# Optimization experiments

Measured on AMD Instinct MI355X. Metric: run time of the kernel, lower is better.

The kernel has to match this reference:

```python
import jax, jax.numpy as jnp
import numpy as np

N_SRC, N_TGT, N_EDGES = 100000, 50000, 600000
IN_CH, OUT_CH = 128, 128
NUM_EDGE_TYPES, NUM_NODE_TYPES = 7, 4


def setup_inputs() -> dict:
    key = jax.random.key(0)
    ks = jax.random.split(key, 9)
    x_src = jax.random.normal(ks[0], (N_SRC, IN_CH), dtype=jnp.float32)
    x_target = jax.random.normal(ks[1], (N_TGT, IN_CH), dtype=jnp.float32)
    # PyG Linear: y = x @ W.T (+ b); W has shape (out, in)
    rel_w = jax.random.normal(ks[2], (NUM_EDGE_TYPES, OUT_CH, IN_CH), dtype=jnp.float32) * 0.05
    root_w = jax.random.normal(ks[3], (NUM_NODE_TYPES, OUT_CH, IN_CH), dtype=jnp.float32) * 0.05
    root_b = jax.random.normal(ks[4], (NUM_NODE_TYPES, OUT_CH), dtype=jnp.float32) * 0.05
    edge_src = jax.random.randint(ks[5], (N_EDGES,), 0, N_SRC, dtype=jnp.int32)
    edge_dst = jax.random.randint(ks[6], (N_EDGES,), 0, N_TGT, dtype=jnp.int32)
    edge_type = jax.random.randint(ks[7], (N_EDGES,), 0, NUM_EDGE_TYPES, dtype=jnp.int32)
    target_node_type = jax.random.randint(ks[8], (N_TGT,), 0, NUM_NODE_TYPES, dtype=jnp.int32)
    return {
        "x_src": x_src, "x_target": x_target,
        "rel_w": rel_w, "root_w": root_w, "root_b": root_b,
        "edge_src": edge_src, "edge_dst": edge_dst,
        "edge_type": edge_type, "target_node_type": target_node_type,
    }


def reference(x_src, x_target, rel_w, root_w, root_b,
              edge_src, edge_dst, edge_type, target_node_type):
    n_tgt = x_target.shape[0]
    num_rel = rel_w.shape[0]
    num_ntypes = root_w.shape[0]
    # Gather source features once for all edges: (E, in)
    msg = x_src[edge_src]
    out = jnp.zeros((n_tgt, rel_w.shape[1]), dtype=x_target.dtype)
    # Per-relation linear transform + scatter-MEAN over that relation's edges
    # (matches one propagate(aggr='mean') call per edge type: nodes with no
    #  incoming edges of type r contribute 0 for that relation).
    for r in range(num_rel):
        mask = (edge_type == r).astype(msg.dtype)  # (E,)
        y = (msg * mask[:, None]) @ rel_w[r].T     # (E, out)
        s = jax.ops.segment_sum(y, edge_dst, num_segments=n_tgt)
        cnt = jax.ops.segment_sum(mask, edge_dst, num_segments=n_tgt)
        out = out + s / jnp.maximum(cnt, 1.0)[:, None]
    # Per-node-type root linear (with bias), masked add
    for t in range(num_ntypes):
        m = (target_node_type == t)
        root = x_target @ root_w[t].T + root_b[t]
        out = out + jnp.where(m[:, None], root, 0.0)
    return out
```

## Files before the change

kernel.cpp:

```cpp
#include <hip/hip_runtime.h>

#define NSRC 100000
#define NTGT 50000
#define NE   600000
#define CH   128
#define NREL 7
#define NTYP 4
#define NP   (NREL * NTGT)
#define NB   ((NP + 1023) / 1024)
#define NBLK (NTGT / 16)

typedef __attribute__((ext_vector_type(4))) float f32x4;
typedef __attribute__((ext_vector_type(8))) short bf16x8;
typedef unsigned int uint;
typedef unsigned short ushort;

static constexpr long long NXB4 = (long long)NSRC * CH / 4;
static constexpr long long NXT4 = (long long)NTGT * CH / 4;
static constexpr long long NWR4 = (long long)NREL * CH * CH / 4;
static constexpr long long NWT4 = (long long)NTYP * CH * CH / 4;
static constexpr int CONVB  = (int)((NXB4 + NXT4 + NWR4 + NWT4 + 255) / 256);
static constexpr int COUNTB = (NE + 255) / 256;

static constexpr size_t A256(size_t x) { return (x + 255) & ~(size_t)255; }
static constexpr size_t CNT_O   = 0;
static constexpr size_t BSE_O   = A256(CNT_O + (size_t)NP * 4);
static constexpr size_t EOFF_O  = A256(BSE_O + (size_t)NB * 4);
static constexpr size_t CUR_O   = A256(EOFF_O + (size_t)(NP + 1) * 4);
static constexpr size_t SEDGE_O = A256(CUR_O + (size_t)NP * 4);
static constexpr size_t WB_O    = A256(SEDGE_O + (size_t)NE * 4);
static constexpr size_t XB_O    = A256(WB_O + (size_t)(NREL + NTYP) * CH * CH * 2);
static constexpr size_t XTB_O   = A256(XB_O + (size_t)NSRC * CH * 2);

#define GLOAD_LDS(gp, lp) __builtin_amdgcn_global_load_lds( \
    (const __attribute__((address_space(1))) void*)(gp), \
    (__attribute__((address_space(3))) void*)(lp), 16, 0, 0)
#define FENCE_VM()   asm volatile("s_waitcnt vmcnt(0)" ::: "memory")
#define FENCE_FULL() asm volatile("s_waitcnt vmcnt(0) lgkmcnt(0)" ::: "memory")

__device__ __forceinline__ uint bfpack(float a, float b) {
  uint ua = __float_as_uint(a); ua = (ua + 0x7fff + ((ua >> 16) & 1)) >> 16;
  uint ub = __float_as_uint(b); ub = (ub + 0x7fff + ((ub >> 16) & 1)) >> 16;
  return ua | (ub << 16);
}
__device__ __forceinline__ ushort f2b(float x) {
  uint u = __float_as_uint(x);
  return (ushort)((u + 0x7fff + ((u >> 16) & 1)) >> 16);
}
__device__ __forceinline__ float bl(uint u) { return __uint_as_float(u << 16); }
__device__ __forceinline__ float bh(uint u) { return __uint_as_float(u & 0xffff0000u); }

__global__ __launch_bounds__(256) void k_count(const int* __restrict__ edst,
                                               const int* __restrict__ etyp,
                                               int* __restrict__ cnt) {
  int i = blockIdx.x * 256 + threadIdx.x;
  if (i < NE) atomicAdd(&cnt[etyp[i] * NTGT + edst[i]], 1);
}

__global__ __launch_bounds__(256) void k_s1(const int* __restrict__ cnt,
                                            int* __restrict__ bsE) {
  __shared__ int sE[256];
  int t = threadIdx.x, p0 = blockIdx.x * 1024 + t * 4;
  int e = 0;
#pragma unroll
  for (int j = 0; j < 4; ++j) {
    int p = p0 + j;
    if (p < NP) e += cnt[p];
  }
  sE[t] = e; __syncthreads();
  for (int s = 128; s > 0; s >>= 1) {
    if (t < s) sE[t] += sE[t + s];
    __syncthreads();
  }
  if (t == 0) bsE[blockIdx.x] = sE[0];
}

__global__ __launch_bounds__(512) void k_s23(const int* __restrict__ cnt,
                                             const int* __restrict__ bsE,
                                             int* __restrict__ eoff,
                                             int* __restrict__ cur) {
  __shared__ int sE[512];
  __shared__ int sBase;
  int t = threadIdx.x;
  int e = (t < NB) ? bsE[t] : 0;
  sE[t] = e; __syncthreads();
  for (int s = 1; s < 512; s <<= 1) {
    int a = 0; if (t >= s) a = sE[t - s];
    __syncthreads();
    sE[t] += a;
    __syncthreads();
  }
  if (t == blockIdx.x) sBase = sE[t] - e;
  __syncthreads();
  int base0 = sBase;
  int p0 = blockIdx.x * 1024 + t * 2;
  int c0 = (p0 < NP) ? cnt[p0] : 0;
  int c1 = (p0 + 1 < NP) ? cnt[p0 + 1] : 0;
  int e2 = c0 + c1;
  sE[t] = e2; __syncthreads();
  for (int s = 1; s < 512; s <<= 1) {
    int a = 0; if (t >= s) a = sE[t - s];
    __syncthreads();
    sE[t] += a;
    __syncthreads();
  }
  int baseE = base0 + sE[t] - e2;
  if (p0 < NP)     { eoff[p0] = baseE;          cur[p0] = baseE; }
  if (p0 + 1 < NP) { eoff[p0 + 1] = baseE + c0; cur[p0 + 1] = baseE + c0; }
  if (p0 + 1 == NP - 1) eoff[NP] = baseE + c0 + c1;
}

__global__ __launch_bounds__(256) void k_esconv(
    const int* __restrict__ esrc, const int* __restrict__ edst,
    const int* __restrict__ etyp, int* __restrict__ cur, int* __restrict__ sedge,
    const float* __restrict__ xsrc, const float* __restrict__ xt,
    const float* __restrict__ relw, const float* __restrict__ rootw,
    ushort* __restrict__ xb, ushort* __restrict__ xtb, ushort* __restrict__ wb) {
  int bx = blockIdx.x;
  if (bx < COUNTB) {
    int i = bx * 256 + threadIdx.x;
    if (i < NE) {
      int p = etyp[i] * NTGT + edst[i];
      int pos = atomicAdd(&cur[p], 1);
      sedge[pos] = esrc[i];
    }
    return;
  }
  bx -= COUNTB;
  long long i4 = (long long)bx * 256 + threadIdx.x;
  const float* src; ushort* dst; long long off;
  if (i4 < NXB4) { src = xsrc; dst = xb; off = i4; }
  else if (i4 < NXB4 + NXT4) { src = xt; dst = xtb; off = i4 - NXB4; }
  else if (i4 < NXB4 + NXT4 + NWR4) { src = relw; dst = wb; off = i4 - NXB4 - NXT4; }
  else if (i4 < NXB4 + NXT4 + NWR4 + NWT4) {
    src = rootw; dst = wb + (size_t)NREL * CH * CH; off = i4 - NXB4 - NXT4 - NWR4;
  } else return;
  float4 v = *(const float4*)(src + off * 4);
  uint lo = (uint)f2b(v.x) | ((uint)f2b(v.y) << 16);
  uint hi = (uint)f2b(v.z) | ((uint)f2b(v.w) << 16);
  uint2 o = make_uint2(lo, hi);
  *(uint2*)(dst + off * 4) = o;
}

__device__ __forceinline__ void mfma_acc(const ushort* strip, const ushort* W,
                                         int m, int quad, f32x4* acc) {
  bf16x8 aF[4];
#pragma unroll
  for (int ks = 0; ks < 4; ++ks) {
    int c = ks * 4 + quad;
    aF[ks] = *(const bf16x8*)&strip[(m * 16 + (c ^ m)) << 3];
  }
#pragma unroll
  for (int ct = 0; ct < 8; ++ct) {
    int n = ct * 16 + m;
#pragma unroll
    for (int ks = 0; ks < 4; ++ks) {
      bf16x8 bF = *(const bf16x8*)(W + (size_t)n * CH + ks * 32 + quad * 8);
      acc[ct] = __builtin_amdgcn_mfma_f32_16x16x32_bf16(aF[ks], bF, acc[ct], 0, 0, 0);
    }
  }
}

__global__ __launch_bounds__(64) void k_mega(const ushort* __restrict__ xb,
    const ushort* __restrict__ xtb, const ushort* __restrict__ wb,
    const int* __restrict__ eoff, const int* __restrict__ sedge,
    const int* __restrict__ ntyp, const float* __restrict__ rootb,
    float* __restrict__ out) {
  __shared__ ushort As[16 * CH];
  int ln = threadIdx.x;
  int m = ln & 15, quad = ln >> 4;
  int dstbase = blockIdx.x * 16;

  int lc = min(ln, 16);
  int evr[NREL];
#pragma unroll
  for (int r = 0; r < NREL; ++r)
    evr[r] = eoff[r * NTGT + dstbase + lc];
  int nv = ntyp[dstbase + min(ln, 15)];
  uint xr[16];
#pragma unroll
  for (int i = 0; i < 16; ++i)
    xr[i] = *(const uint*)(xtb + (size_t)(dstbase + i) * CH + (ln << 1));

  f32x4 acc[8];
#pragma unroll
  for (int ct = 0; ct < 8; ++ct) acc[ct] = (f32x4){0.f, 0.f, 0.f, 0.f};

#pragma unroll
  for (int rel = 0; rel < NREL; ++rel) {
    int ev = evr[rel];
    int e0 = __builtin_amdgcn_readlane(ev, 0);
    int e1 = __builtin_amdgcn_readlane(ev, 16);
    if (e1 <= e0) continue;

    float aRx[16], aRy[16];
#pragma unroll
    for (int i = 0; i < 16; ++i) { aRx[i] = 0.f; aRy[i] = 0.f; }

    for (int cb = e0; cb < e1; cb += 16) {
      int nc = e1 - cb; if (nc > 16) nc = 16;
      int ng = (nc + 3) >> 2;
      uint ai[4];
      int esl = cb + (ln >> 4);
#pragma unroll
      for (int g = 0; g < 4; ++g) {
        if (g < ng) {
          int e = esl + g * 4;
          if (e > e1 - 1) e = e1 - 1;
          ai[g] = (uint)sedge[e];
        }
      }
      FENCE_FULL();
#pragma unroll
      for (int g = 0; g < 4; ++g) {
        if (g < ng) {
          const ushort* gp = xb + (size_t)ai[g] * CH + ((ln & 15) << 3);
          GLOAD_LDS(gp, &As[g << 9]);
        }
      }
      FENCE_VM();
#pragma unroll
      for (int i = 0; i < 16; ++i) {
        int lo = __builtin_amdgcn_readlane(ev, i);
        int hi = __builtin_amdgcn_readlane(ev, i + 1);
        if (lo < cb) lo = cb;
        int ce = cb + nc; if (hi > ce) hi = ce;
        for (int e = lo; e < hi; ++e) {
          uint u = *(const uint*)&As[((e - cb) << 7) + (ln << 1)];
          aRx[i] += bl(u);
          aRy[i] += bh(u);
        }
      }
    }

#pragma unroll
    for (int i = 0; i < 16; ++i) {
      int n = __builtin_amdgcn_readlane(ev, i + 1) - __builtin_amdgcn_readlane(ev, i);
      float inv = (n > 0) ? __builtin_amdgcn_rcpf((float)n) : 0.f;
      uint w = bfpack(aRx[i] * inv, aRy[i] * inv);
      int c = ln >> 2;
      *(uint*)&As[((i * 16 + (c ^ i)) << 3) + ((ln & 3) << 1)] = w;
    }
    mfma_acc(As, wb + (size_t)rel * CH * CH, m, quad, acc);
  }

#pragma unroll
  for (int ty = 0; ty < NTYP; ++ty) {
#pragma unroll
    for (int i = 0; i < 16; ++i) {
      int nti = __builtin_amdgcn_readlane(nv, i);
      uint w = (nti == ty) ? xr[i] : 0u;
      int c = ln >> 2;
      *(uint*)&As[((i * 16 + (c ^ i)) << 3) + ((ln & 3) << 1)] = w;
    }
    mfma_acc(As, wb + (size_t)(NREL + ty) * CH * CH, m, quad, acc);
  }

#pragma unroll
  for (int reg = 0; reg < 4; ++reg) {
    int row = quad * 4 + reg;
    int dst = dstbase + row;
    int tt = ntyp[dst];
    const float* rb = rootb + (size_t)tt * CH;
#pragma unroll
    for (int ct = 0; ct < 8; ++ct) {
      int col = ct * 16 + m;
      out[(size_t)dst * CH + col] = acc[ct][reg] + rb[col];
    }
  }
}

extern "C" void kernel_launch(void* const* d_in, const int* in_sizes, int n_in,
                              void* d_out, int out_size, void* d_ws, size_t ws_size,
                              hipStream_t stream) {
  (void)in_sizes; (void)n_in; (void)out_size; (void)ws_size;
  const float* xsrc  = (const float*)d_in[0];
  const float* xt    = (const float*)d_in[1];
  const float* relw  = (const float*)d_in[2];
  const float* rootw = (const float*)d_in[3];
  const float* rootb = (const float*)d_in[4];
  const int* esrc = (const int*)d_in[5];
  const int* edst = (const int*)d_in[6];
  const int* etyp = (const int*)d_in[7];
  const int* ntyp = (const int*)d_in[8];
  float* out = (float*)d_out;

  char* ws = (char*)d_ws;
  int*   cnt    = (int*)(ws + CNT_O);
  int*   bsE    = (int*)(ws + BSE_O);
  int*   eoff   = (int*)(ws + EOFF_O);
  int*   cur    = (int*)(ws + CUR_O);
  int*   sedge  = (int*)(ws + SEDGE_O);
  ushort* wb    = (ushort*)(ws + WB_O);
  ushort* xb    = (ushort*)(ws + XB_O);
  ushort* xtb   = (ushort*)(ws + XTB_O);

  hipMemsetAsync(cnt, 0, (size_t)NP * 4, stream);
  k_count<<<dim3(COUNTB), dim3(256), 0, stream>>>(edst, etyp, cnt);
  k_s1<<<dim3(NB), dim3(256), 0, stream>>>(cnt, bsE);
  k_s23<<<dim3(NB), dim3(512), 0, stream>>>(cnt, bsE, eoff, cur);
  k_esconv<<<dim3(COUNTB + CONVB), dim3(256), 0, stream>>>(
      esrc, edst, etyp, cur, sedge, xsrc, xt, relw, rootw, xb, xtb, wb);
  k_mega<<<dim3(NBLK), dim3(64), 0, stream>>>(
      xb, xtb, wb, eoff, sedge, ntyp, rootb, out);
}
```

Measured before the change: 403.4 us.

## Gather edge messages into sorted bf16 buffer and stream them with double buffering

Drops the full bf16 conversion of x_src. A new gather kernel reads each edge's fp32 source row, converts it to bf16 and writes it into a dst/type-sorted message buffer at the slot claimed by the atomic. The main kernel then reads contiguous message chunks through double-buffered global-to-LDS loads with partial vmcnt waits, instead of indirect row loads that fully serialize. Blocks now run two waves, the x_target/weight conversion is merged into the count kernel, and the x_target row loads move after the relation loop. The cost is writing and re-reading a 600k-row bf16 message buffer, plus more LDS per block.

```diff
diff --git a/kernel.cpp b/kernel.cpp
--- a/kernel.cpp
+++ b/kernel.cpp
@@ -8,35 +8,35 @@
 #define NTYP 4
 #define NP   (NREL * NTGT)
 #define NB   ((NP + 1023) / 1024)
-#define NBLK (NTGT / 16)
+#define NBLK ((NTGT + 31) / 32)
 
 typedef __attribute__((ext_vector_type(4))) float f32x4;
 typedef __attribute__((ext_vector_type(8))) short bf16x8;
 typedef unsigned int uint;
 typedef unsigned short ushort;
 
-static constexpr long long NXB4 = (long long)NSRC * CH / 4;
 static constexpr long long NXT4 = (long long)NTGT * CH / 4;
 static constexpr long long NWR4 = (long long)NREL * CH * CH / 4;
 static constexpr long long NWT4 = (long long)NTYP * CH * CH / 4;
-static constexpr int CONVB  = (int)((NXB4 + NXT4 + NWR4 + NWT4 + 255) / 256);
+static constexpr int CONVB  = (int)((NXT4 + NWR4 + NWT4 + 255) / 256);
 static constexpr int COUNTB = (NE + 255) / 256;
+static constexpr int GATB   = NE / 16;
 
 static constexpr size_t A256(size_t x) { return (x + 255) & ~(size_t)255; }
 static constexpr size_t CNT_O   = 0;
 static constexpr size_t BSE_O   = A256(CNT_O + (size_t)NP * 4);
 static constexpr size_t EOFF_O  = A256(BSE_O + (size_t)NB * 4);
 static constexpr size_t CUR_O   = A256(EOFF_O + (size_t)(NP + 1) * 4);
-static constexpr size_t SEDGE_O = A256(CUR_O + (size_t)NP * 4);
-static constexpr size_t WB_O    = A256(SEDGE_O + (size_t)NE * 4);
-static constexpr size_t XB_O    = A256(WB_O + (size_t)(NREL + NTYP) * CH * CH * 2);
-static constexpr size_t XTB_O   = A256(XB_O + (size_t)NSRC * CH * 2);
+static constexpr size_t WB_O    = A256(CUR_O + (size_t)NP * 4);
+static constexpr size_t XTB_O   = A256(WB_O + (size_t)(NREL + NTYP) * CH * CH * 2);
+static constexpr size_t MSG_O   = A256(XTB_O + (size_t)NTGT * CH * 2);
 
 #define GLOAD_LDS(gp, lp) __builtin_amdgcn_global_load_lds( \
     (const __attribute__((address_space(1))) void*)(gp), \
     (__attribute__((address_space(3))) void*)(lp), 16, 0, 0)
-#define FENCE_VM()   asm volatile("s_waitcnt vmcnt(0)" ::: "memory")
-#define FENCE_FULL() asm volatile("s_waitcnt vmcnt(0) lgkmcnt(0)" ::: "memory")
+#define WAITVM4()   asm volatile("s_waitcnt vmcnt(4)" ::: "memory")
+#define WAITVM0()   asm volatile("s_waitcnt vmcnt(0)" ::: "memory")
+#define WAITLGKM0() asm volatile("s_waitcnt lgkmcnt(0)" ::: "memory")
 
 __device__ __forceinline__ uint bfpack(float a, float b) {
   uint ua = __float_as_uint(a); ua = (ua + 0x7fff + ((ua >> 16) & 1)) >> 16;
@@ -50,10 +50,30 @@
 __device__ __forceinline__ float bl(uint u) { return __uint_as_float(u << 16); }
 __device__ __forceinline__ float bh(uint u) { return __uint_as_float(u & 0xffff0000u); }
 
-__global__ __launch_bounds__(256) void k_count(const int* __restrict__ edst,
-                                               const int* __restrict__ etyp,
-                                               int* __restrict__ cnt) {
-  int i = blockIdx.x * 256 + threadIdx.x;
+__global__ __launch_bounds__(256) void k_pre(
+    const float* __restrict__ xt, const float* __restrict__ relw,
+    const float* __restrict__ rootw, ushort* __restrict__ xtb,
+    ushort* __restrict__ wb,
+    const int* __restrict__ edst, const int* __restrict__ etyp,
+    int* __restrict__ cnt) {
+  int bx = blockIdx.x;
+  if (bx < CONVB) {
+    long long i4 = (long long)bx * 256 + threadIdx.x;
+    const float* src; ushort* dst; long long off;
+    if (i4 < NXT4) { src = xt; dst = xtb; off = i4; }
+    else if (i4 < NXT4 + NWR4) { src = relw; dst = wb; off = i4 - NXT4; }
+    else if (i4 < NXT4 + NWR4 + NWT4) {
+      src = rootw; dst = wb + (size_t)NREL * CH * CH; off = i4 - NXT4 - NWR4;
+    } else return;
+    float4 v = *(const float4*)(src + off * 4);
+    uint lo = (uint)f2b(v.x) | ((uint)f2b(v.y) << 16);
+    uint hi = (uint)f2b(v.z) | ((uint)f2b(v.w) << 16);
+    uint2 o = make_uint2(lo, hi);
+    *(uint2*)(dst + off * 4) = o;
+    return;
+  }
+  bx -= CONVB;
+  int i = bx * 256 + threadIdx.x;
   if (i < NE) atomicAdd(&cnt[etyp[i] * NTGT + edst[i]], 1);
 }
 
@@ -110,36 +130,25 @@
   if (p0 + 1 == NP - 1) eoff[NP] = baseE + c0 + c1;
 }
 
-__global__ __launch_bounds__(256) void k_esconv(
-    const int* __restrict__ esrc, const int* __restrict__ edst,
-    const int* __restrict__ etyp, int* __restrict__ cur, int* __restrict__ sedge,
-    const float* __restrict__ xsrc, const float* __restrict__ xt,
-    const float* __restrict__ relw, const float* __restrict__ rootw,
-    ushort* __restrict__ xb, ushort* __restrict__ xtb, ushort* __restrict__ wb) {
-  int bx = blockIdx.x;
-  if (bx < COUNTB) {
-    int i = bx * 256 + threadIdx.x;
-    if (i < NE) {
-      int p = etyp[i] * NTGT + edst[i];
-      int pos = atomicAdd(&cur[p], 1);
-      sedge[pos] = esrc[i];
-    }
-    return;
-  }
-  bx -= COUNTB;
-  long long i4 = (long long)bx * 256 + threadIdx.x;
-  const float* src; ushort* dst; long long off;
-  if (i4 < NXB4) { src = xsrc; dst = xb; off = i4; }
-  else if (i4 < NXB4 + NXT4) { src = xt; dst = xtb; off = i4 - NXB4; }
-  else if (i4 < NXB4 + NXT4 + NWR4) { src = relw; dst = wb; off = i4 - NXB4 - NXT4; }
-  else if (i4 < NXB4 + NXT4 + NWR4 + NWT4) {
-    src = rootw; dst = wb + (size_t)NREL * CH * CH; off = i4 - NXB4 - NXT4 - NWR4;
-  } else return;
-  float4 v = *(const float4*)(src + off * 4);
-  uint lo = (uint)f2b(v.x) | ((uint)f2b(v.y) << 16);
-  uint hi = (uint)f2b(v.z) | ((uint)f2b(v.w) << 16);
-  uint2 o = make_uint2(lo, hi);
-  *(uint2*)(dst + off * 4) = o;
+__global__ __launch_bounds__(256) void k_gat(
+    const float* __restrict__ xsrc, const int* __restrict__ esrc,
+    const int* __restrict__ edst, const int* __restrict__ etyp,
+    int* __restrict__ cur, ushort* __restrict__ msg) {
+  int tid = threadIdx.x;
+  int e = blockIdx.x * 16 + (tid >> 4);
+  int l16 = tid & 15;
+  int src = esrc[e];
+  int p = etyp[e] * NTGT + edst[e];
+  int pos = 0;
+  if (l16 == 0) pos = atomicAdd(&cur[p], 1);
+  pos = __shfl(pos, (tid & 63) & ~15);
+  const float* rp = xsrc + (size_t)src * CH + l16 * 8;
+  float4 v0 = *(const float4*)rp;
+  float4 v1 = *(const float4*)(rp + 4);
+  uint4 o;
+  o.x = bfpack(v0.x, v0.y); o.y = bfpack(v0.z, v0.w);
+  o.z = bfpack(v1.x, v1.y); o.w = bfpack(v1.z, v1.w);
+  *(uint4*)(msg + (size_t)pos * CH + l16 * 8) = o;
 }
 
 __device__ __forceinline__ void mfma_acc(const ushort* strip, const ushort* W,
@@ -161,32 +170,37 @@
   }
 }
 
-__global__ __launch_bounds__(64) void k_mega(const ushort* __restrict__ xb,
+__global__ __launch_bounds__(128) void k_mega(const ushort* __restrict__ msg,
     const ushort* __restrict__ xtb, const ushort* __restrict__ wb,
-    const int* __restrict__ eoff, const int* __restrict__ sedge,
-    const int* __restrict__ ntyp, const float* __restrict__ rootb,
-    float* __restrict__ out) {
-  __shared__ ushort As[16 * CH];
-  int ln = threadIdx.x;
+    const int* __restrict__ eoff, const int* __restrict__ ntyp,
+    const float* __restrict__ rootb, float* __restrict__ out) {
+  __shared__ ushort As[2 * 6144];
+  int wv = threadIdx.x >> 6, ln = threadIdx.x & 63;
+  ushort* Wbuf = As + wv * 6144;
+  ushort* strip = Wbuf + 4096;
   int m = ln & 15, quad = ln >> 4;
-  int dstbase = blockIdx.x * 16;
+  int dstbase = blockIdx.x * 32 + wv * 16;
+  if (dstbase >= NTGT) return;
 
   int lc = min(ln, 16);
   int evr[NREL];
 #pragma unroll
   for (int r = 0; r < NREL; ++r)
     evr[r] = eoff[r * NTGT + dstbase + lc];
-  int nv = ntyp[dstbase + min(ln, 15)];
-  uint xr[16];
-#pragma unroll
-  for (int i = 0; i < 16; ++i)
-    xr[i] = *(const uint*)(xtb + (size_t)(dstbase + i) * CH + (ln << 1));
 
   f32x4 acc[8];
 #pragma unroll
   for (int ct = 0; ct < 8; ++ct) acc[ct] = (f32x4){0.f, 0.f, 0.f, 0.f};
 
-#pragma unroll
+#define STAGE(k) do { \
+    const ushort* gp = msg + (size_t)(e0 + (k) * 16) * CH + (size_t)(ln * 8); \
+    ushort* lb = Wbuf + ((k) & 1) * 2048; \
+    GLOAD_LDS(gp, lb); \
+    GLOAD_LDS(gp + 4 * CH, lb + 512); \
+    GLOAD_LDS(gp + 8 * CH, lb + 1024); \
+    GLOAD_LDS(gp + 12 * CH, lb + 1536); \
+  } while (0)
+
   for (int rel = 0; rel < NREL; ++rel) {
     int ev = evr[rel];
     int e0 = __builtin_amdgcn_readlane(ev, 0);
@@ -197,36 +211,23 @@
 #pragma unroll
     for (int i = 0; i < 16; ++i) { aRx[i] = 0.f; aRy[i] = 0.f; }
 
-    for (int cb = e0; cb < e1; cb += 16) {
-      int nc = e1 - cb; if (nc > 16) nc = 16;
-      int ng = (nc + 3) >> 2;
-      uint ai[4];
-      int esl = cb + (ln >> 4);
-#pragma unroll
-      for (int g = 0; g < 4; ++g) {
-        if (g < ng) {
-          int e = esl + g * 4;
-          if (e > e1 - 1) e = e1 - 1;
-          ai[g] = (uint)sedge[e];
-        }
-      }
-      FENCE_FULL();
-#pragma unroll
-      for (int g = 0; g < 4; ++g) {
-        if (g < ng) {
-          const ushort* gp = xb + (size_t)ai[g] * CH + ((ln & 15) << 3);
-          GLOAD_LDS(gp, &As[g << 9]);
-        }
-      }
-      FENCE_VM();
+    int nchunk = (e1 - e0 + 15) >> 4;
+    WAITLGKM0();
+    STAGE(0);
+    for (int k = 0; k < nchunk; ++k) {
+      if (k + 1 < nchunk) { STAGE(k + 1); WAITVM4(); }
+      else               { WAITVM0(); }
+      const ushort* buf = Wbuf + (k & 1) * 2048;
+      int cb = e0 + k * 16;
+      int ce = cb + 16; if (ce > e1) ce = e1;
 #pragma unroll
       for (int i = 0; i < 16; ++i) {
         int lo = __builtin_amdgcn_readlane(ev, i);
         int hi = __builtin_amdgcn_readlane(ev, i + 1);
         if (lo < cb) lo = cb;
-        int ce = cb + nc; if (hi > ce) hi = ce;
+        if (hi > ce) hi = ce;
         for (int e = lo; e < hi; ++e) {
-          uint u = *(const uint*)&As[((e - cb) << 7) + (ln << 1)];
+          uint u = *(const uint*)&buf[((e - cb) << 7) + (ln << 1)];
           aRx[i] += bl(u);
           aRy[i] += bh(u);
         }
@@ -239,11 +240,17 @@
       float inv = (n > 0) ? __builtin_amdgcn_rcpf((float)n) : 0.f;
       uint w = bfpack(aRx[i] * inv, aRy[i] * inv);
       int c = ln >> 2;
-      *(uint*)&As[((i * 16 + (c ^ i)) << 3) + ((ln & 3) << 1)] = w;
-    }
-    mfma_acc(As, wb + (size_t)rel * CH * CH, m, quad, acc);
-  }
-
+      *(uint*)&strip[((i * 16 + (c ^ i)) << 3) + ((ln & 3) << 1)] = w;
+    }
+    mfma_acc(strip, wb + (size_t)rel * CH * CH, m, quad, acc);
+  }
+#undef STAGE
+
+  int nv = ntyp[dstbase + min(ln, 15)];
+  uint xr[16];
+#pragma unroll
+  for (int i = 0; i < 16; ++i)
+    xr[i] = *(const uint*)(xtb + (size_t)(dstbase + i) * CH + (ln << 1));
 #pragma unroll
   for (int ty = 0; ty < NTYP; ++ty) {
 #pragma unroll
@@ -251,9 +258,9 @@
       int nti = __builtin_amdgcn_readlane(nv, i);
       uint w = (nti == ty) ? xr[i] : 0u;
       int c = ln >> 2;
-      *(uint*)&As[((i * 16 + (c ^ i)) << 3) + ((ln & 3) << 1)] = w;
-    }
-    mfma_acc(As, wb + (size_t)(NREL + ty) * CH * CH, m, quad, acc);
+      *(uint*)&strip[((i * 16 + (c ^ i)) << 3) + ((ln & 3) << 1)] = w;
+    }
+    mfma_acc(strip, wb + (size_t)(NREL + ty) * CH * CH, m, quad, acc);
   }
 
 #pragma unroll
@@ -290,17 +297,16 @@
   int*   bsE    = (int*)(ws + BSE_O);
   int*   eoff   = (int*)(ws + EOFF_O);
   int*   cur    = (int*)(ws + CUR_O);
-  int*   sedge  = (int*)(ws + SEDGE_O);
   ushort* wb    = (ushort*)(ws + WB_O);
-  ushort* xb    = (ushort*)(ws + XB_O);
   ushort* xtb   = (ushort*)(ws + XTB_O);
+  ushort* msg   = (ushort*)(ws + MSG_O);
 
   hipMemsetAsync(cnt, 0, (size_t)NP * 4, stream);
-  k_count<<<dim3(COUNTB), dim3(256), 0, stream>>>(edst, etyp, cnt);
+  k_pre<<<dim3(CONVB + COUNTB), dim3(256), 0, stream>>>(
+      xt, relw, rootw, xtb, wb, edst, etyp, cnt);
   k_s1<<<dim3(NB), dim3(256), 0, stream>>>(cnt, bsE);
   k_s23<<<dim3(NB), dim3(512), 0, stream>>>(cnt, bsE, eoff, cur);
-  k_esconv<<<dim3(COUNTB + CONVB), dim3(256), 0, stream>>>(
-      esrc, edst, etyp, cur, sedge, xsrc, xt, relw, rootw, xb, xtb, wb);
-  k_mega<<<dim3(NBLK), dim3(64), 0, stream>>>(
-      xb, xtb, wb, eoff, sedge, ntyp, rootb, out);
-}
+  k_gat<<<dim3(GATB), dim3(256), 0, stream>>>(xsrc, esrc, edst, etyp, cur, msg);
+  k_mega<<<dim3(NBLK), dim3(128), 0, stream>>>(
+      msg, xtb, wb, eoff, ntyp, rootb, out);
+}
```

Measured after the change: 383.1 us. 1.05x faster.

## Split fused aggregate+GEMM kernel into separate mean-aggregation and MFMA GEMM kernels

Applied to the files above, without the earlier changes.

Replaces the single 64-thread-per-block mega kernel with two stages. A gather kernel computes per-(relation,target) bf16 means, with 16 lanes per segment and 16 segments per block. A GEMM kernel then runs four waves per block, each wave covering half the output columns of a 16-row tile, loading A tiles through LDS. The fp32-to-bf16 conversion moves into the counting kernel so the edge sort runs alone. The aim is to remove the serialized per-row readlane loops and low occupancy of the fused kernel, at the cost of writing and re-reading a 7×50000×128 bf16 intermediate.

```diff
diff --git a/kernel.cpp b/kernel.cpp
--- a/kernel.cpp
+++ b/kernel.cpp
@@ -8,7 +8,8 @@
 #define NTYP 4
 #define NP   (NREL * NTGT)
 #define NB   ((NP + 1023) / 1024)
-#define NBLK (NTGT / 16)
+#define AGGB (NP / 16)
+#define GEMB 1563
 
 typedef __attribute__((ext_vector_type(4))) float f32x4;
 typedef __attribute__((ext_vector_type(8))) short bf16x8;
@@ -31,12 +32,14 @@
 static constexpr size_t WB_O    = A256(SEDGE_O + (size_t)NE * 4);
 static constexpr size_t XB_O    = A256(WB_O + (size_t)(NREL + NTYP) * CH * CH * 2);
 static constexpr size_t XTB_O   = A256(XB_O + (size_t)NSRC * CH * 2);
+static constexpr size_t MEAN_O  = A256(XTB_O + (size_t)NTGT * CH * 2);
 
 #define GLOAD_LDS(gp, lp) __builtin_amdgcn_global_load_lds( \
     (const __attribute__((address_space(1))) void*)(gp), \
     (__attribute__((address_space(3))) void*)(lp), 16, 0, 0)
-#define FENCE_VM()   asm volatile("s_waitcnt vmcnt(0)" ::: "memory")
-#define FENCE_FULL() asm volatile("s_waitcnt vmcnt(0) lgkmcnt(0)" ::: "memory")
+#define WAITVM0()   asm volatile("s_waitcnt vmcnt(0)" ::: "memory")
+#define WAITLGKM0() asm volatile("s_waitcnt lgkmcnt(0)" ::: "memory")
+#define SB0()       __builtin_amdgcn_sched_barrier(0)
 
 __device__ __forceinline__ uint bfpack(float a, float b) {
   uint ua = __float_as_uint(a); ua = (ua + 0x7fff + ((ua >> 16) & 1)) >> 16;
@@ -50,10 +53,31 @@
 __device__ __forceinline__ float bl(uint u) { return __uint_as_float(u << 16); }
 __device__ __forceinline__ float bh(uint u) { return __uint_as_float(u & 0xffff0000u); }
 
-__global__ __launch_bounds__(256) void k_count(const int* __restrict__ edst,
-                                               const int* __restrict__ etyp,
-                                               int* __restrict__ cnt) {
-  int i = blockIdx.x * 256 + threadIdx.x;
+__global__ __launch_bounds__(256) void k_pre(
+    const float* __restrict__ xsrc, const float* __restrict__ xt,
+    const float* __restrict__ relw, const float* __restrict__ rootw,
+    ushort* __restrict__ xb, ushort* __restrict__ xtb, ushort* __restrict__ wb,
+    const int* __restrict__ edst, const int* __restrict__ etyp,
+    int* __restrict__ cnt) {
+  int bx = blockIdx.x;
+  if (bx < CONVB) {
+    long long i4 = (long long)bx * 256 + threadIdx.x;
+    const float* src; ushort* dst; long long off;
+    if (i4 < NXB4) { src = xsrc; dst = xb; off = i4; }
+    else if (i4 < NXB4 + NXT4) { src = xt; dst = xtb; off = i4 - NXB4; }
+    else if (i4 < NXB4 + NXT4 + NWR4) { src = relw; dst = wb; off = i4 - NXB4 - NXT4; }
+    else if (i4 < NXB4 + NXT4 + NWR4 + NWT4) {
+      src = rootw; dst = wb + (size_t)NREL * CH * CH; off = i4 - NXB4 - NXT4 - NWR4;
+    } else return;
+    float4 v = *(const float4*)(src + off * 4);
+    uint lo = (uint)f2b(v.x) | ((uint)f2b(v.y) << 16);
+    uint hi = (uint)f2b(v.z) | ((uint)f2b(v.w) << 16);
+    uint2 o = make_uint2(lo, hi);
+    *(uint2*)(dst + off * 4) = o;
+    return;
+  }
+  bx -= CONVB;
+  int i = bx * 256 + threadIdx.x;
   if (i < NE) atomicAdd(&cnt[etyp[i] * NTGT + edst[i]], 1);
 }
 
@@ -110,150 +134,131 @@
   if (p0 + 1 == NP - 1) eoff[NP] = baseE + c0 + c1;
 }
 
-__global__ __launch_bounds__(256) void k_esconv(
+__global__ __launch_bounds__(256) void k_esort(
     const int* __restrict__ esrc, const int* __restrict__ edst,
-    const int* __restrict__ etyp, int* __restrict__ cur, int* __restrict__ sedge,
-    const float* __restrict__ xsrc, const float* __restrict__ xt,
-    const float* __restrict__ relw, const float* __restrict__ rootw,
-    ushort* __restrict__ xb, ushort* __restrict__ xtb, ushort* __restrict__ wb) {
-  int bx = blockIdx.x;
-  if (bx < COUNTB) {
-    int i = bx * 256 + threadIdx.x;
-    if (i < NE) {
-      int p = etyp[i] * NTGT + edst[i];
-      int pos = atomicAdd(&cur[p], 1);
-      sedge[pos] = esrc[i];
-    }
-    return;
-  }
-  bx -= COUNTB;
-  long long i4 = (long long)bx * 256 + threadIdx.x;
-  const float* src; ushort* dst; long long off;
-  if (i4 < NXB4) { src = xsrc; dst = xb; off = i4; }
-  else if (i4 < NXB4 + NXT4) { src = xt; dst = xtb; off = i4 - NXB4; }
-  else if (i4 < NXB4 + NXT4 + NWR4) { src = relw; dst = wb; off = i4 - NXB4 - NXT4; }
-  else if (i4 < NXB4 + NXT4 + NWR4 + NWT4) {
-    src = rootw; dst = wb + (size_t)NREL * CH * CH; off = i4 - NXB4 - NXT4 - NWR4;
-  } else return;
-  float4 v = *(const float4*)(src + off * 4);
-  uint lo = (uint)f2b(v.x) | ((uint)f2b(v.y) << 16);
-  uint hi = (uint)f2b(v.z) | ((uint)f2b(v.w) << 16);
-  uint2 o = make_uint2(lo, hi);
-  *(uint2*)(dst + off * 4) = o;
-}
-
-__device__ __forceinline__ void mfma_acc(const ushort* strip, const ushort* W,
-                                         int m, int quad, f32x4* acc) {
-  bf16x8 aF[4];
+    const int* __restrict__ etyp, int* __restrict__ cur,
+    int* __restrict__ sedge) {
+  int i = blockIdx.x * 256 + threadIdx.x;
+  if (i < NE) {
+    int p = etyp[i] * NTGT + edst[i];
+    int pos = atomicAdd(&cur[p], 1);
+    sedge[pos] = esrc[i];
+  }
+}
+
+__global__ __launch_bounds__(256) void k_agg(
+    const ushort* __restrict__ xb, const int* __restrict__ sedge,
+    const int* __restrict__ eoff, ushort* __restrict__ mean) {
+  int tid = threadIdx.x;
+  int g = tid >> 4, l16 = tid & 15;
+  int p = blockIdx.x * 16 + g;
+  int lo = eoff[p], hi = eoff[p + 1];
+  int cnt = hi - lo;
+  float acc[8];
+#pragma unroll
+  for (int c = 0; c < 8; ++c) acc[c] = 0.f;
+  int base = lo;
+  while (base < hi) {
+    int nb = hi - base; if (nb > 16) nb = 16;
+    int sv = (l16 < nb) ? sedge[base + l16] : 0;
+    for (int j = 0; j < nb; ++j) {
+      int s = __shfl(sv, (g & 3) * 16 + j);
+      uint4 v = *(const uint4*)(xb + (size_t)s * CH + (l16 << 3));
+      acc[0] += bl(v.x); acc[1] += bh(v.x);
+      acc[2] += bl(v.y); acc[3] += bh(v.y);
+      acc[4] += bl(v.z); acc[5] += bh(v.z);
+      acc[6] += bl(v.w); acc[7] += bh(v.w);
+    }
+    base += 16;
+  }
+  float inv = (cnt > 0) ? __builtin_amdgcn_rcpf((float)cnt) : 0.f;
+  uint4 o;
+  o.x = bfpack(acc[0] * inv, acc[1] * inv);
+  o.y = bfpack(acc[2] * inv, acc[3] * inv);
+  o.z = bfpack(acc[4] * inv, acc[5] * inv);
+  o.w = bfpack(acc[6] * inv, acc[7] * inv);
+  *(uint4*)(mean + (size_t)p * CH + (l16 << 3)) = o;
+}
+
+__global__ __launch_bounds__(256) void k_gemm(
+    const ushort* __restrict__ mean, const ushort* __restrict__ xtb,
+    const ushort* __restrict__ wb, const int* __restrict__ ntyp,
+    const float* __restrict__ rootb, float* __restrict__ out) {
+  __shared__ ushort As[4 * 2048];
+  int wv = threadIdx.x >> 6, ln = threadIdx.x & 63;
+  ushort* strip = As + wv * 2048;
+  int m = ln & 15, quad = ln >> 4;
+  int w = blockIdx.x * 4 + wv;
+  int tile = w >> 1, half = w & 1;
+  int dstbase = tile * 16;
+  if (dstbase >= NTGT) return;
+  int ct0 = half * 4;
+
+  f32x4 acc[4];
+#pragma unroll
+  for (int ct = 0; ct < 4; ++ct) acc[ct] = (f32x4){0.f, 0.f, 0.f, 0.f};
+
+  for (int ph = 0; ph < NREL; ++ph) {
+    const ushort* gb = mean + ((size_t)ph * NTGT + dstbase) * CH;
+    WAITLGKM0(); SB0();
+#pragma unroll
+    for (int t4 = 0; t4 < 4; ++t4) {
+      int i = t4 * 4 + quad;
+      const ushort* gp = gb + (size_t)i * CH + ((m ^ i) << 3);
+      GLOAD_LDS(gp, strip + t4 * 512);
+    }
+    WAITVM0(); SB0();
+    bf16x8 aF[4];
+#pragma unroll
+    for (int ks = 0; ks < 4; ++ks) {
+      int c = ks * 4 + quad;
+      aF[ks] = *(const bf16x8*)&strip[(m * 16 + (c ^ m)) << 3];
+    }
+    const ushort* W = wb + (size_t)ph * CH * CH;
+#pragma unroll
+    for (int ct = 0; ct < 4; ++ct) {
+      int n = (ct0 + ct) * 16 + m;
+#pragma unroll
+      for (int ks = 0; ks < 4; ++ks) {
+        bf16x8 bF = *(const bf16x8*)(W + (size_t)n * CH + ks * 32 + quad * 8);
+        acc[ct] = __builtin_amdgcn_mfma_f32_16x16x32_bf16(aF[ks], bF, acc[ct], 0, 0, 0);
+      }
+    }
+  }
+
+  WAITLGKM0(); SB0();
+#pragma unroll
+  for (int t4 = 0; t4 < 4; ++t4) {
+    int i = t4 * 4 + quad;
+    const ushort* gp = xtb + (size_t)(dstbase + i) * CH + ((m ^ i) << 3);
+    GLOAD_LDS(gp, strip + t4 * 512);
+  }
+  WAITVM0(); SB0();
+  int myt = ntyp[dstbase + m];
+  union { uint u[4]; bf16x8 v; } aT[4];
 #pragma unroll
   for (int ks = 0; ks < 4; ++ks) {
     int c = ks * 4 + quad;
-    aF[ks] = *(const bf16x8*)&strip[(m * 16 + (c ^ m)) << 3];
-  }
-#pragma unroll
-  for (int ct = 0; ct < 8; ++ct) {
-    int n = ct * 16 + m;
-#pragma unroll
-    for (int ks = 0; ks < 4; ++ks) {
-      bf16x8 bF = *(const bf16x8*)(W + (size_t)n * CH + ks * 32 + quad * 8);
-      acc[ct] = __builtin_amdgcn_mfma_f32_16x16x32_bf16(aF[ks], bF, acc[ct], 0, 0, 0);
-    }
-  }
-}
-
-__global__ __launch_bounds__(64) void k_mega(const ushort* __restrict__ xb,
-    const ushort* __restrict__ xtb, const ushort* __restrict__ wb,
-    const int* __restrict__ eoff, const int* __restrict__ sedge,
-    const int* __restrict__ ntyp, const float* __restrict__ rootb,
-    float* __restrict__ out) {
-  __shared__ ushort As[16 * CH];
-  int ln = threadIdx.x;
-  int m = ln & 15, quad = ln >> 4;
-  int dstbase = blockIdx.x * 16;
-
-  int lc = min(ln, 16);
-  int evr[NREL];
-#pragma unroll
-  for (int r = 0; r < NREL; ++r)
-    evr[r] = eoff[r * NTGT + dstbase + lc];
-  int nv = ntyp[dstbase + min(ln, 15)];
-  uint xr[16];
-#pragma unroll
-  for (int i = 0; i < 16; ++i)
-    xr[i] = *(const uint*)(xtb + (size_t)(dstbase + i) * CH + (ln << 1));
-
-  f32x4 acc[8];
-#pragma unroll
-  for (int ct = 0; ct < 8; ++ct) acc[ct] = (f32x4){0.f, 0.f, 0.f, 0.f};
-
-#pragma unroll
-  for (int rel = 0; rel < NREL; ++rel) {
-    int ev = evr[rel];
-    int e0 = __builtin_amdgcn_readlane(ev, 0);
-    int e1 = __builtin_amdgcn_readlane(ev, 16);
-    if (e1 <= e0) continue;
-
-    float aRx[16], aRy[16];
-#pragma unroll
-    for (int i = 0; i < 16; ++i) { aRx[i] = 0.f; aRy[i] = 0.f; }
-
-    for (int cb = e0; cb < e1; cb += 16) {
-      int nc = e1 - cb; if (nc > 16) nc = 16;
-      int ng = (nc + 3) >> 2;
-      uint ai[4];
-      int esl = cb + (ln >> 4);
-#pragma unroll
-      for (int g = 0; g < 4; ++g) {
-        if (g < ng) {
-          int e = esl + g * 4;
-          if (e > e1 - 1) e = e1 - 1;
-          ai[g] = (uint)sedge[e];
-        }
+    aT[ks].v = *(const bf16x8*)&strip[(m * 16 + (c ^ m)) << 3];
+  }
+#pragma unroll
+  for (int ty = 0; ty < NTYP; ++ty) {
+    union { uint u[4]; bf16x8 v; } aM[4];
+#pragma unroll
+    for (int ks = 0; ks < 4; ++ks)
+#pragma unroll
+      for (int k2 = 0; k2 < 4; ++k2)
+        aM[ks].u[k2] = (myt == ty) ? aT[ks].u[k2] : 0u;
+    const ushort* W = wb + (size_t)(NREL + ty) * CH * CH;
+#pragma unroll
+    for (int ct = 0; ct < 4; ++ct) {
+      int n = (ct0 + ct) * 16 + m;
+#pragma unroll
+      for (int ks = 0; ks < 4; ++ks) {
+        bf16x8 bF = *(const bf16x8*)(W + (size_t)n * CH + ks * 32 + quad * 8);
+        acc[ct] = __builtin_amdgcn_mfma_f32_16x16x32_bf16(aM[ks].v, bF, acc[ct], 0, 0, 0);
       }
-      FENCE_FULL();
-#pragma unroll
-      for (int g = 0; g < 4; ++g) {
-        if (g < ng) {
-          const ushort* gp = xb + (size_t)ai[g] * CH + ((ln & 15) << 3);
-          GLOAD_LDS(gp, &As[g << 9]);
-        }
-      }
-      FENCE_VM();
-#pragma unroll
-      for (int i = 0; i < 16; ++i) {
-        int lo = __builtin_amdgcn_readlane(ev, i);
-        int hi = __builtin_amdgcn_readlane(ev, i + 1);
-        if (lo < cb) lo = cb;
-        int ce = cb + nc; if (hi > ce) hi = ce;
-        for (int e = lo; e < hi; ++e) {
-          uint u = *(const uint*)&As[((e - cb) << 7) + (ln << 1)];
-          aRx[i] += bl(u);
-          aRy[i] += bh(u);
-        }
-      }
-    }
-
-#pragma unroll
-    for (int i = 0; i < 16; ++i) {
-      int n = __builtin_amdgcn_readlane(ev, i + 1) - __builtin_amdgcn_readlane(ev, i);
-      float inv = (n > 0) ? __builtin_amdgcn_rcpf((float)n) : 0.f;
-      uint w = bfpack(aRx[i] * inv, aRy[i] * inv);
-      int c = ln >> 2;
-      *(uint*)&As[((i * 16 + (c ^ i)) << 3) + ((ln & 3) << 1)] = w;
-    }
-    mfma_acc(As, wb + (size_t)rel * CH * CH, m, quad, acc);
-  }
-
-#pragma unroll
-  for (int ty = 0; ty < NTYP; ++ty) {
-#pragma unroll
-    for (int i = 0; i < 16; ++i) {
-      int nti = __builtin_amdgcn_readlane(nv, i);
-      uint w = (nti == ty) ? xr[i] : 0u;
-      int c = ln >> 2;
-      *(uint*)&As[((i * 16 + (c ^ i)) << 3) + ((ln & 3) << 1)] = w;
-    }
-    mfma_acc(As, wb + (size_t)(NREL + ty) * CH * CH, m, quad, acc);
+    }
   }
 
 #pragma unroll
@@ -263,8 +268,8 @@
     int tt = ntyp[dst];
     const float* rb = rootb + (size_t)tt * CH;
 #pragma unroll
-    for (int ct = 0; ct < 8; ++ct) {
-      int col = ct * 16 + m;
+    for (int ct = 0; ct < 4; ++ct) {
+      int col = (ct0 + ct) * 16 + m;
       out[(size_t)dst * CH + col] = acc[ct][reg] + rb[col];
     }
   }
@@ -294,13 +299,15 @@
   ushort* wb    = (ushort*)(ws + WB_O);
   ushort* xb    = (ushort*)(ws + XB_O);
   ushort* xtb   = (ushort*)(ws + XTB_O);
+  ushort* mean  = (ushort*)(ws + MEAN_O);
 
   hipMemsetAsync(cnt, 0, (size_t)NP * 4, stream);
-  k_count<<<dim3(COUNTB), dim3(256), 0, stream>>>(edst, etyp, cnt);
+  k_pre<<<dim3(CONVB + COUNTB), dim3(256), 0, stream>>>(
+      xsrc, xt, relw, rootw, xb, xtb, wb, edst, etyp, cnt);
   k_s1<<<dim3(NB), dim3(256), 0, stream>>>(cnt, bsE);
   k_s23<<<dim3(NB), dim3(512), 0, stream>>>(cnt, bsE, eoff, cur);
-  k_esconv<<<dim3(COUNTB + CONVB), dim3(256), 0, stream>>>(
-      esrc, edst, etyp, cur, sedge, xsrc, xt, relw, rootw, xb, xtb, wb);
-  k_mega<<<dim3(NBLK), dim3(64), 0, stream>>>(
-      xb, xtb, wb, eoff, sedge, ntyp, rootb, out);
-}
+  k_esort<<<dim3(COUNTB), dim3(256), 0, stream>>>(esrc, edst, etyp, cur, sedge);
+  k_agg<<<dim3(AGGB), dim3(256), 0, stream>>>(xb, sedge, eoff, mean);
+  k_gemm<<<dim3(GEMB), dim3(256), 0, stream>>>(
+      mean, xtb, wb, ntyp, rootb, out);
+}
```

New measurement: 392.5 us. -2.7%, faster.
